# Kernel optimization log

Hardware: AMD Instinct MI355X
Metric: run time of the kernel (lower is better)

## Reference

```python
import jax, jax.numpy as jnp
import numpy as np

N, CIN, T, V = 16, 16, 512, 200
K, COUT, H = 3, 64, 64


def setup_inputs() -> dict:
    key = jax.random.key(0)
    ks = jax.random.split(key, 9)
    s = 0.05
    return {
        "x": jax.random.normal(ks[0], (N, CIN, T, V), jnp.float32),
        "A": jax.random.uniform(ks[1], (K, V, V), jnp.float32) / V,
        "W_gcn": jax.random.normal(ks[2], (K * COUT, CIN), jnp.float32) * s,
        "b_gcn": jnp.zeros((K * COUT,), jnp.float32),
        "W_ih": jax.random.normal(ks[3], (4 * H, COUT), jnp.float32) * s,
        "W_hh": jax.random.normal(ks[4], (4 * H, H), jnp.float32) * s,
        "b_ih": jnp.zeros((4 * H,), jnp.float32),
        "b_hh": jnp.zeros((4 * H,), jnp.float32),
        "W_fc": jax.random.normal(ks[5], (1, H), jnp.float32) * s,
        "b_fc": jnp.zeros((1,), jnp.float32),
    }


def reference(x, A, W_gcn, b_gcn, W_ih, W_hh, b_ih, b_hh, W_fc, b_fc):
    n, c, t, v = x.shape
    k = A.shape[0]
    cout = W_gcn.shape[0] // k
    # ConvTemporalGraphical: 1x1 conv -> (n, k*cout, t, v), reshape, adjacency einsum
    y = jnp.einsum('nctv,oc->notv', x, W_gcn) + b_gcn[None, :, None, None]
    y = y.reshape(n, k, cout, t, v)
    y = jnp.einsum('nkctv,kvw->nctw', y, A)  # (n, cout, t, v)
    # mean over node dim, residual=False -> res=0
    y = jnp.mean(y, axis=3)  # (n, cout, t)
    seq = jnp.transpose(y, (2, 0, 1))  # (t, n, cout) time-major for scan

    def step(carry, xt):
        h, ccell = carry
        gates = xt @ W_ih.T + b_ih + h @ W_hh.T + b_hh  # (n, 4H)
        i, f, g, o = jnp.split(gates, 4, axis=-1)  # torch LSTM gate order
        i = jax.nn.sigmoid(i)
        f = jax.nn.sigmoid(f)
        g = jnp.tanh(g)
        o = jax.nn.sigmoid(o)
        ccell = f * ccell + i * g
        h = o * jnp.tanh(ccell)
        return (h, ccell), None

    h0 = jnp.zeros((n, W_hh.shape[1]), x.dtype)
    (h_last, _), _ = jax.lax.scan(step, (h0, h0), seq)
    out = h_last @ W_fc.T + b_fc  # (n, 1)
    return (out, A)
```

## Files before the change

### kernel.cpp

```cpp
#include <hip/hip_runtime.h>
#include <math.h>

#define N_    16
#define CIN_  16
#define T_    512
#define V_    200
#define K_    3
#define COUT_ 64
#define H_    64
#define G_    256

#define WS_A  0
#define WS_SA 640
#define WS_XA 1024
#define WS_XW (WS_XA + N_ * T_ * K_ * CIN_)

typedef __attribute__((ext_vector_type(4))) float f32x4;

__device__ __forceinline__ float fast_sig(float x) {
    return __builtin_amdgcn_rcpf(1.f + __expf(-x));
}
__device__ __forceinline__ float fast_tanh(float x) {
    return fmaf(-2.f, __builtin_amdgcn_rcpf(1.f + __expf(2.f * x)), 1.f);
}

#define NCOPY ((K_ * V_ * V_ + 255) / 256)
__global__ __launch_bounds__(256) void prep_kernel(const float* __restrict__ A,
                                                   float* __restrict__ out,
                                                   float* __restrict__ ws) {
    int b = blockIdx.x;
    if (b < NCOPY) {
        int tid = b * 256 + threadIdx.x;
        if (tid < K_ * V_ * V_) out[16 + tid] = A[tid];
        if (tid < K_ * V_) {
            const float* row = A + (long)tid * V_;
            float s = 0.f;
            for (int w = 0; w < V_; ++w) s += row[w];
            ws[WS_A + tid] = s * (1.0f / V_);
        }
    } else {
        int k = b - NCOPY;
        const float* Ak = A + (long)k * V_ * V_;
        float s = 0.f;
        for (int i = threadIdx.x; i < V_ * V_; i += 256) s += Ak[i];
        #pragma unroll
        for (int m = 1; m < 64; m <<= 1) s += __shfl_xor(s, m);
        __shared__ float red[4];
        if ((threadIdx.x & 63) == 0) red[threadIdx.x >> 6] = s;
        __syncthreads();
        if (threadIdx.x == 0)
            ws[WS_SA + k] = (red[0] + red[1] + red[2] + red[3]) * (1.0f / V_);
    }
}

#define TT 64
#define PADV 204
__global__ __launch_bounds__(256) void xa_kernel(const float* __restrict__ x,
                                                 float* __restrict__ ws) {
    __shared__ __align__(16) float xt[TT * PADV];
    __shared__ __align__(16) float aS[K_ * V_];
    int tid = threadIdx.x;
    int b = blockIdx.x;
    int tchunk = b & 7;
    int ci = (b >> 3) & 15;
    int n = b >> 7;
    int t0 = tchunk * TT;

    for (int i = tid; i < K_ * V_; i += 256) aS[i] = ws[WS_A + i];

    const float4* xg4 =
        (const float4*)(x + ((long)(n * CIN_ + ci) * T_ + t0) * V_);
    for (int j = tid; j < TT * (V_ / 4); j += 256) {
        float4 v = xg4[j];
        int t = j / (V_ / 4), v4 = (j % (V_ / 4)) * 4;
        *(float4*)(xt + t * PADV + v4) = v;
    }
    __syncthreads();

    int t_local = tid & 63;
    int k = tid >> 6;
    if (k < K_) {
        const float* xr = xt + t_local * PADV;
        const float* ar = aS + k * V_;
        float a0 = 0.f, a1 = 0.f, a2 = 0.f, a3 = 0.f;
        #pragma unroll 5
        for (int v4 = 0; v4 < V_; v4 += 4) {
            float4 xv = *(const float4*)(xr + v4);
            float4 av = *(const float4*)(ar + v4);
            a0 = fmaf(xv.x, av.x, a0);
            a1 = fmaf(xv.y, av.y, a1);
            a2 = fmaf(xv.z, av.z, a2);
            a3 = fmaf(xv.w, av.w, a3);
        }
        float s = (a0 + a1) + (a2 + a3);
        ws[WS_XA + ((long)n * T_ + (t0 + t_local)) * (K_ * CIN_) + k * CIN_ + ci] = s;
    }
}

__global__ __launch_bounds__(256) void seqgates_kernel(
    const float* __restrict__ W_gcn, const float* __restrict__ b_gcn,
    const float* __restrict__ W_ih, const float* __restrict__ b_ih,
    const float* __restrict__ b_hh, float* __restrict__ ws) {
    int t = blockIdx.x;
    int tid = threadIdx.x;
    __shared__ float xaS[N_][K_ * CIN_];
    __shared__ __align__(16) float seqS[N_][COUT_];
    __shared__ float saS[K_];

    if (tid < K_) saS[tid] = ws[WS_SA + tid];
    #pragma unroll
    for (int r = 0; r < 3; ++r) {
        int i = tid + r * 256;
        if (i < N_ * K_ * CIN_) {
            int n = i / (K_ * CIN_), kc = i % (K_ * CIN_);
            xaS[n][kc] = ws[WS_XA + (long)(n * T_ + t) * (K_ * CIN_) + kc];
        }
    }
    __syncthreads();

    {
        int n = tid >> 4, c0 = (tid & 15) * 4;
        #pragma unroll
        for (int cc = 0; cc < 4; ++cc) {
            int c = c0 + cc;
            float s = 0.f;
            #pragma unroll
            for (int k = 0; k < K_; ++k) {
                s = fmaf(b_gcn[k * COUT_ + c], saS[k], s);
                const float* wrow = W_gcn + (long)(k * COUT_ + c) * CIN_;
                #pragma unroll
                for (int ci = 0; ci < CIN_; ++ci)
                    s = fmaf(wrow[ci], xaS[n][k * CIN_ + ci], s);
            }
            seqS[n][c] = s;
        }
    }
    __syncthreads();

    {
        int g = tid;
        float acc[N_];
        #pragma unroll
        for (int n = 0; n < N_; ++n) acc[n] = 0.f;
        const float4* wrow4 = (const float4*)(W_ih + (long)g * H_);
        #pragma unroll
        for (int c4 = 0; c4 < H_ / 4; ++c4) {
            float4 w4 = wrow4[c4];
            #pragma unroll
            for (int n = 0; n < N_; ++n) {
                float4 s4 = ((const float4*)seqS[n])[c4];
                acc[n] = fmaf(w4.x, s4.x, acc[n]);
                acc[n] = fmaf(w4.y, s4.y, acc[n]);
                acc[n] = fmaf(w4.z, s4.z, acc[n]);
                acc[n] = fmaf(w4.w, s4.w, acc[n]);
            }
        }
        float bias = b_ih[g] + b_hh[g];
        #pragma unroll
        for (int n = 0; n < N_; ++n)
            ws[WS_XW + (long)(t * N_ + n) * G_ + g] = acc[n] + bias;
    }
}

__global__ __launch_bounds__(256, 1) void lstm_kernel(
    const float* __restrict__ W_hh, const float* __restrict__ W_fc,
    const float* __restrict__ b_fc, const float* __restrict__ ws,
    float* __restrict__ out) {
    int n = blockIdx.x;
    int w = threadIdx.x >> 6;
    int lane = threadIdx.x & 63;

    const f32x4* wr = (const f32x4*)(W_hh + (long)(w * H_ + lane) * H_);
    f32x4 w0, w1, w2, w3, w4, w5, w6, w7, w8, w9, w10, w11, w12, w13, w14, w15;
    #define WLOAD(i) \
        asm volatile("global_load_dwordx4 %0, %1, off" : "=v"(w##i) : "v"(wr + i));
    WLOAD(0)  WLOAD(1)  WLOAD(2)  WLOAD(3)
    WLOAD(4)  WLOAD(5)  WLOAD(6)  WLOAD(7)
    WLOAD(8)  WLOAD(9)  WLOAD(10) WLOAD(11)
    WLOAD(12) WLOAD(13) WLOAD(14) WLOAD(15)
    #undef WLOAD
    asm volatile("s_waitcnt vmcnt(0)" ::: "memory");

    __shared__ __align__(16) float hS[H_];
    __shared__ float gbuf[4][H_];

    if (threadIdx.x < H_) hS[threadIdx.x] = 0.f;
    float ccell = 0.f, hlast = 0.f;
    __syncthreads();

    const float* xw = ws + WS_XW + (long)n * G_ + (w * H_ + lane);
    float x0 = xw[0];
    float x1 = xw[(long)N_ * G_];

    for (int t = 0; t < T_; ++t) {
        float gate = x0;
        x0 = x1;
        if (t + 2 < T_) x1 = xw[(long)(t + 2) * N_ * G_];

        float a0 = 0.f, a1 = 0.f, a2 = 0.f, a3 = 0.f;
        const float4* h4 = (const float4*)hS;
        #define DOT4(i)                            \
            {                                      \
                float4 hv = h4[i];                 \
                a0 = fmaf(w##i[0], hv.x, a0);      \
                a1 = fmaf(w##i[1], hv.y, a1);      \
                a2 = fmaf(w##i[2], hv.z, a2);      \
                a3 = fmaf(w##i[3], hv.w, a3);      \
            }
        DOT4(0)  DOT4(1)  DOT4(2)  DOT4(3)
        DOT4(4)  DOT4(5)  DOT4(6)  DOT4(7)
        DOT4(8)  DOT4(9)  DOT4(10) DOT4(11)
        DOT4(12) DOT4(13) DOT4(14) DOT4(15)
        #undef DOT4
        gate += (a0 + a1) + (a2 + a3);

        gbuf[w][lane] = gate;
        __syncthreads();
        if (w == 0) {
            float iv = fast_sig(gate);
            float fv = fast_sig(gbuf[1][lane]);
            float gv = fast_tanh(gbuf[2][lane]);
            float ov = fast_sig(gbuf[3][lane]);
            ccell = fmaf(fv, ccell, iv * gv);
            hlast = ov * fast_tanh(ccell);
            hS[lane] = hlast;
        }
        __syncthreads();
    }

    if (w == 0) {
        float p = hlast * W_fc[lane];
        #pragma unroll
        for (int m = 1; m < 64; m <<= 1) p += __shfl_xor(p, m);
        if (lane == 0) out[n] = p + b_fc[0];
    }
}

extern "C" void kernel_launch(void* const* d_in, const int* in_sizes, int n_in,
                              void* d_out, int out_size, void* d_ws, size_t ws_size,
                              hipStream_t stream) {
    const float* x     = (const float*)d_in[0];
    const float* A     = (const float*)d_in[1];
    const float* W_gcn = (const float*)d_in[2];
    const float* b_gcn = (const float*)d_in[3];
    const float* W_ih  = (const float*)d_in[4];
    const float* W_hh  = (const float*)d_in[5];
    const float* b_ih  = (const float*)d_in[6];
    const float* b_hh  = (const float*)d_in[7];
    const float* W_fc  = (const float*)d_in[8];
    const float* b_fc  = (const float*)d_in[9];
    float* out = (float*)d_out;
    float* ws  = (float*)d_ws;

    prep_kernel<<<NCOPY + K_, 256, 0, stream>>>(A, out, ws);
    xa_kernel<<<N_ * CIN_ * (T_ / TT), 256, 0, stream>>>(x, ws);
    seqgates_kernel<<<T_, 256, 0, stream>>>(W_gcn, b_gcn, W_ih, b_ih, b_hh, ws);
    lstm_kernel<<<N_, 256, 0, stream>>>(W_hh, W_fc, b_fc, ws, out);
}
```

Before: 353.9 us.

## Fold adjacency prep into xa kernel and move A copy into seqgates

```diff
diff --git a/kernel.cpp b/kernel.cpp
--- a/kernel.cpp
+++ b/kernel.cpp
@@ -10,7 +10,6 @@
 #define H_    64
 #define G_    256
 
-#define WS_A  0
 #define WS_SA 640
 #define WS_XA 1024
 #define WS_XW (WS_XA + N_ * T_ * K_ * CIN_)
@@ -24,85 +23,91 @@
     return fmaf(-2.f, __builtin_amdgcn_rcpf(1.f + __expf(2.f * x)), 1.f);
 }
 
-#define NCOPY ((K_ * V_ * V_ + 255) / 256)
-__global__ __launch_bounds__(256) void prep_kernel(const float* __restrict__ A,
-                                                   float* __restrict__ out,
-                                                   float* __restrict__ ws) {
-    int b = blockIdx.x;
-    if (b < NCOPY) {
-        int tid = b * 256 + threadIdx.x;
-        if (tid < K_ * V_ * V_) out[16 + tid] = A[tid];
-        if (tid < K_ * V_) {
-            const float* row = A + (long)tid * V_;
-            float s = 0.f;
-            for (int w = 0; w < V_; ++w) s += row[w];
-            ws[WS_A + tid] = s * (1.0f / V_);
-        }
-    } else {
-        int k = b - NCOPY;
-        const float* Ak = A + (long)k * V_ * V_;
-        float s = 0.f;
-        for (int i = threadIdx.x; i < V_ * V_; i += 256) s += Ak[i];
-        #pragma unroll
-        for (int m = 1; m < 64; m <<= 1) s += __shfl_xor(s, m);
-        __shared__ float red[4];
-        if ((threadIdx.x & 63) == 0) red[threadIdx.x >> 6] = s;
-        __syncthreads();
-        if (threadIdx.x == 0)
-            ws[WS_SA + k] = (red[0] + red[1] + red[2] + red[3]) * (1.0f / V_);
-    }
-}
-
 #define TT 64
 #define PADV 204
-__global__ __launch_bounds__(256) void xa_kernel(const float* __restrict__ x,
-                                                 float* __restrict__ ws) {
+__global__ __launch_bounds__(256) void xa2_kernel(const float* __restrict__ x,
+                                                  const float* __restrict__ A,
+                                                  float* __restrict__ ws) {
+    int b = blockIdx.x;
+    int tid = threadIdx.x;
+
+    if (b == 256) {
+        int k = tid >> 6, lane = tid & 63;
+        if (k < K_) {
+            const float* Ak = A + (long)k * V_ * V_;
+            float s = 0.f;
+            for (int i = lane; i < V_ * V_; i += 64) s += Ak[i];
+            #pragma unroll
+            for (int m = 1; m < 64; m <<= 1) s += __shfl_xor(s, m);
+            if (lane == 0) ws[WS_SA + k] = s * (1.0f / V_);
+        }
+        return;
+    }
+
     __shared__ __align__(16) float xt[TT * PADV];
     __shared__ __align__(16) float aS[K_ * V_];
-    int tid = threadIdx.x;
-    int b = blockIdx.x;
-    int tchunk = b & 7;
-    int ci = (b >> 3) & 15;
-    int n = b >> 7;
-    int t0 = tchunk * TT;
-
-    for (int i = tid; i < K_ * V_; i += 256) aS[i] = ws[WS_A + i];
-
-    const float4* xg4 =
-        (const float4*)(x + ((long)(n * CIN_ + ci) * T_ + t0) * V_);
-    for (int j = tid; j < TT * (V_ / 4); j += 256) {
-        float4 v = xg4[j];
-        int t = j / (V_ / 4), v4 = (j % (V_ / 4)) * 4;
-        *(float4*)(xt + t * PADV + v4) = v;
+    int n = b >> 4, ci = b & 15;
+
+    for (int r = tid; r < K_ * V_; r += 256) {
+        const float4* row = (const float4*)(A + (long)r * V_);
+        float s0 = 0.f, s1 = 0.f, s2 = 0.f, s3 = 0.f;
+        #pragma unroll 10
+        for (int j = 0; j < V_ / 4; ++j) {
+            float4 v = row[j];
+            s0 += v.x; s1 += v.y; s2 += v.z; s3 += v.w;
+        }
+        aS[r] = ((s0 + s1) + (s2 + s3)) * (1.0f / V_);
     }
     __syncthreads();
 
     int t_local = tid & 63;
     int k = tid >> 6;
-    if (k < K_) {
-        const float* xr = xt + t_local * PADV;
-        const float* ar = aS + k * V_;
-        float a0 = 0.f, a1 = 0.f, a2 = 0.f, a3 = 0.f;
-        #pragma unroll 5
-        for (int v4 = 0; v4 < V_; v4 += 4) {
-            float4 xv = *(const float4*)(xr + v4);
-            float4 av = *(const float4*)(ar + v4);
-            a0 = fmaf(xv.x, av.x, a0);
-            a1 = fmaf(xv.y, av.y, a1);
-            a2 = fmaf(xv.z, av.z, a2);
-            a3 = fmaf(xv.w, av.w, a3);
-        }
-        float s = (a0 + a1) + (a2 + a3);
-        ws[WS_XA + ((long)n * T_ + (t0 + t_local)) * (K_ * CIN_) + k * CIN_ + ci] = s;
+
+    for (int tc = 0; tc < T_ / TT; ++tc) {
+        int t0 = tc * TT;
+        const float4* xg4 =
+            (const float4*)(x + ((long)(n * CIN_ + ci) * T_ + t0) * V_);
+        for (int j = tid; j < TT * (V_ / 4); j += 256) {
+            float4 v = xg4[j];
+            int t = j / (V_ / 4), v4 = (j % (V_ / 4)) * 4;
+            *(float4*)(xt + t * PADV + v4) = v;
+        }
+        __syncthreads();
+
+        if (k < K_) {
+            const float* xr = xt + t_local * PADV;
+            const float* ar = aS + k * V_;
+            float a0 = 0.f, a1 = 0.f, a2 = 0.f, a3 = 0.f;
+            #pragma unroll 5
+            for (int v4 = 0; v4 < V_; v4 += 4) {
+                float4 xv = *(const float4*)(xr + v4);
+                float4 av = *(const float4*)(ar + v4);
+                a0 = fmaf(xv.x, av.x, a0);
+                a1 = fmaf(xv.y, av.y, a1);
+                a2 = fmaf(xv.z, av.z, a2);
+                a3 = fmaf(xv.w, av.w, a3);
+            }
+            float s = (a0 + a1) + (a2 + a3);
+            ws[WS_XA + ((long)n * T_ + (t0 + t_local)) * (K_ * CIN_) +
+               k * CIN_ + ci] = s;
+        }
+        __syncthreads();
     }
 }
 
 __global__ __launch_bounds__(256) void seqgates_kernel(
-    const float* __restrict__ W_gcn, const float* __restrict__ b_gcn,
-    const float* __restrict__ W_ih, const float* __restrict__ b_ih,
-    const float* __restrict__ b_hh, float* __restrict__ ws) {
+    const float* __restrict__ A, const float* __restrict__ W_gcn,
+    const float* __restrict__ b_gcn, const float* __restrict__ W_ih,
+    const float* __restrict__ b_ih, const float* __restrict__ b_hh,
+    float* __restrict__ out, float* __restrict__ ws) {
     int t = blockIdx.x;
     int tid = threadIdx.x;
+
+    {
+        int gid = t * 256 + tid;
+        if (gid < K_ * V_ * V_) out[16 + gid] = A[gid];
+    }
+
     __shared__ float xaS[N_][K_ * CIN_];
     __shared__ __align__(16) float seqS[N_][COUT_];
     __shared__ float saS[K_];
@@ -252,8 +257,8 @@
     float* out = (float*)d_out;
     float* ws  = (float*)d_ws;
 
-    prep_kernel<<<NCOPY + K_, 256, 0, stream>>>(A, out, ws);
-    xa_kernel<<<N_ * CIN_ * (T_ / TT), 256, 0, stream>>>(x, ws);
-    seqgates_kernel<<<T_, 256, 0, stream>>>(W_gcn, b_gcn, W_ih, b_ih, b_hh, ws);
+    xa2_kernel<<<257, 256, 0, stream>>>(x, A, ws);
+    seqgates_kernel<<<T_, 256, 0, stream>>>(A, W_gcn, b_gcn, W_ih, b_ih, b_hh,
+                                            out, ws);
     lstm_kernel<<<N_, 256, 0, stream>>>(W_hh, W_fc, b_fc, ws, out);
 }
```

New measurement: 468.9 us. 32.5% more time.
